# Kernel tuning notes

Measured on AMD Instinct MI355X. Metric: run time of the kernel, lower is better.

The kernel has to match this reference:

```python
import jax, jax.numpy as jnp
import numpy as np

B, T = 16, 512          # batch, timesteps
IN = 16                 # input_path_dim
D = 128                 # cde_state_dim
H = 256                 # vf_hidden_dim
L = 136                 # logsig_size = 16 + 16*15/2 (depth-2 log-signature)
O = 32                  # output_path_dim


def _linear_params(key, out_f, in_f):
    kw, kb = jax.random.split(key)
    lim = 1.0 / np.sqrt(in_f)
    W = jax.random.uniform(kw, (out_f, in_f), minval=-lim, maxval=lim, dtype=jnp.float32)
    b = jax.random.uniform(kb, (out_f,), minval=-lim, maxval=lim, dtype=jnp.float32)
    return W, b


def setup_inputs() -> dict:
    key = jax.random.key(0)
    ks = jax.random.split(key, 10)
    x0 = jax.random.normal(ks[0], (B, IN), dtype=jnp.float32)
    # log-signature increments are small; scale down for numerical realism
    logsigs = jax.random.normal(ks[1], (B, T - 1, L), dtype=jnp.float32) * 0.01
    # initial MLP: IN -> H -> H -> D (softplus activations, linear final)
    iw1, ib1 = _linear_params(ks[2], H, IN)
    iw2, ib2 = _linear_params(ks[3], H, H)
    iw3, ib3 = _linear_params(ks[4], D, H)
    # vector-field MLP: D -> H -> H -> D*L (softplus, tanh final)
    fw1, fb1 = _linear_params(ks[5], H, D)
    fw2, fb2 = _linear_params(ks[6], H, H)
    fw3, fb3 = _linear_params(ks[7], D * L, H)
    # readout: D -> O
    rw, rb = _linear_params(ks[8], O, D)
    return dict(x0=x0, logsigs=logsigs,
                iw1=iw1, ib1=ib1, iw2=iw2, ib2=ib2, iw3=iw3, ib3=ib3,
                fw1=fw1, fb1=fb1, fw2=fw2, fb2=fb2, fw3=fw3, fb3=fb3,
                rw=rw, rb=rb)


def reference(x0, logsigs, iw1, ib1, iw2, ib2, iw3, ib3,
              fw1, fb1, fw2, fb2, fw3, fb3, rw, rb):
    sp = jax.nn.softplus
    # initial MLP -> h0: (B, D)
    h0 = sp(x0 @ iw1.T + ib1)
    h0 = sp(h0 @ iw2.T + ib2)
    h0 = h0 @ iw3.T + ib3

    def step(h, logsig_t):
        # vector-field MLP: (B, D) -> (B, D*L), tanh final activation
        z = sp(h @ fw1.T + fb1)
        z = sp(z @ fw2.T + fb2)
        z = jnp.tanh(z @ fw3.T + fb3)
        mat = z.reshape(h.shape[0], D, L)          # (B, D, L)
        h_next = h + jnp.einsum('bdl,bl->bd', mat, logsig_t)
        return h_next, h_next

    # scan over time: xs shape (T-1, B, L)
    _, h_hist = jax.lax.scan(step, h0, jnp.swapaxes(logsigs, 0, 1))
    h_all = jnp.concatenate([h0[None, :, :], h_hist], axis=0)  # (T, B, D)
    out = h_all @ rw.T + rb                                     # (T, B, O)
    return jnp.swapaxes(out, 0, 1)                              # (B, T, O)
```

## Files before the change

kernel.cpp:

```cpp
#include <hip/hip_runtime.h>

namespace {
constexpr int kB = 16, kT = 512, kIN = 16, kD = 128, kH = 256, kL = 136, kO = 32;
constexpr int kSteps = kT - 1;
constexpr int NBLK = 256;
constexpr int NTHR = 512;
constexpr int LH   = 68;
constexpr int NTILE = 5;
constexpr int OFF_W3L = 0;
constexpr int OFF_AHI = 81920;
constexpr int OFF_ALO = 90368;
constexpr int OFF_DT  = 98816;
constexpr int OFF_OMS = 104192;
constexpr int OFF_Z1S = 108544;
constexpr int OFF_HB  = 109568;
constexpr int OFF_HINC= 110080;
constexpr int OFF_RED = 110592;
constexpr size_t LDS_BYTES = 111104;
}

typedef __attribute__((ext_vector_type(8))) short short8;
typedef __attribute__((ext_vector_type(4))) float f32x4;

__device__ __forceinline__ float softplusf(float x) {
  return fmaxf(x, 0.0f) + log1pf(expf(-fabsf(x)));
}
__device__ __forceinline__ unsigned short f2bf(float x) {
  unsigned u = __float_as_uint(x);
  return (unsigned short)((u + 0x7FFFu + ((u >> 16) & 1u)) >> 16);
}
__device__ __forceinline__ float bf2f(unsigned short h) {
  return __uint_as_float(((unsigned)h) << 16);
}
#define ALOAD64(p)   __hip_atomic_load((p),  __ATOMIC_RELAXED, __HIP_MEMORY_SCOPE_AGENT)
#define ASTORE64(p,v) __hip_atomic_store((p), (v), __ATOMIC_RELAXED, __HIP_MEMORY_SCOPE_AGENT)

__global__ void __launch_bounds__(256)
rde_init(const float* __restrict__ x0,
         const float* __restrict__ iw1, const float* __restrict__ ib1,
         const float* __restrict__ iw2, const float* __restrict__ ib2,
         const float* __restrict__ iw3, const float* __restrict__ ib3,
         float* __restrict__ hist) {
  __shared__ float xs[kIN];
  __shared__ __align__(16) float t1[kH];
  __shared__ __align__(16) float t2[kH];
  const int b = blockIdx.x, tid = threadIdx.x;
  if (tid < kIN) xs[tid] = x0[b*kIN + tid];
  __syncthreads();
  {
    float a = ib1[tid];
#pragma unroll
    for (int i = 0; i < kIN; ++i) a = fmaf(xs[i], iw1[tid*kIN + i], a);
    t1[tid] = softplusf(a);
  }
  __syncthreads();
  {
    const float4* wr = (const float4*)(iw2 + (size_t)tid*kH);
    float a = ib2[tid];
#pragma unroll 8
    for (int q = 0; q < kH/4; ++q) {
      float4 w = wr[q];
      a = fmaf(t1[4*q+0], w.x, a); a = fmaf(t1[4*q+1], w.y, a);
      a = fmaf(t1[4*q+2], w.z, a); a = fmaf(t1[4*q+3], w.w, a);
    }
    t2[tid] = softplusf(a);
  }
  __syncthreads();
  if (tid < kD) {
    const float4* wr = (const float4*)(iw3 + (size_t)tid*kH);
    float a = ib3[tid];
#pragma unroll 8
    for (int q = 0; q < kH/4; ++q) {
      float4 w = wr[q];
      a = fmaf(t2[4*q+0], w.x, a); a = fmaf(t2[4*q+1], w.y, a);
      a = fmaf(t2[4*q+2], w.z, a); a = fmaf(t2[4*q+3], w.w, a);
    }
    hist[(size_t)b*kD + tid] = a;
  }
}

__global__ void __launch_bounds__(NTHR, 2)
rde_scan(const float* __restrict__ lsg,
         const float* __restrict__ fw1, const float* __restrict__ fb1,
         const float* __restrict__ fw2, const float* __restrict__ fb2,
         const float* __restrict__ fw3, const float* __restrict__ fb3,
         float* __restrict__ hist,
         unsigned long long* z2x, unsigned long long* partx) {
  extern __shared__ char smem[];
  unsigned short* W3L = (unsigned short*)(smem + OFF_W3L);
  unsigned short* Ahi = (unsigned short*)(smem + OFF_AHI);
  unsigned short* Alo = (unsigned short*)(smem + OFF_ALO);
  float* Dt   = (float*)(smem + OFF_DT);
  float* oms  = (float*)(smem + OFF_OMS);
  float* z1s  = (float*)(smem + OFF_Z1S);
  float* hb   = (float*)(smem + OFF_HB);
  float* hinc = (float*)(smem + OFF_HINC);
  float* red  = (float*)(smem + OFF_RED);

  const int tid  = threadIdx.x;
  const int k    = blockIdx.x;
  const int wave = tid >> 6, lane = tid & 63;
  const int d_own = k >> 1, l0 = (k & 1) * LH;
  const bool isMLP = (k < kB);
  const int b_own = k;
  const int j = tid >> 1, ksp = tid & 1;

  for (int i = tid; i < NTILE*8*64; i += NTHR) {
    const int w = i >> 9, s = (i >> 6) & 7, ln = i & 63;
    const int nl = w*16 + (ln & 15), g = ln >> 4;
    unsigned hi4[4], lo4[4];
    if (nl < LH) {
      const float* wrow = fw3 + ((size_t)d_own*kL + l0 + nl)*kH + s*32 + g*8;
#pragma unroll
      for (int e = 0; e < 4; ++e) {
        float v0 = wrow[2*e], v1 = wrow[2*e+1];
        unsigned short h0 = f2bf(v0), h1 = f2bf(v1);
        unsigned short l0_ = f2bf(v0 - bf2f(h0)), l1_ = f2bf(v1 - bf2f(h1));
        hi4[e] = (unsigned)h0 | ((unsigned)h1 << 16);
        lo4[e] = (unsigned)l0_ | ((unsigned)l1_ << 16);
      }
    } else {
#pragma unroll
      for (int e = 0; e < 4; ++e) { hi4[e] = 0u; lo4[e] = 0u; }
    }
    unsigned* dh = (unsigned*)(W3L + (((w*8+s)*2+0)*64 + ln)*8);
    unsigned* dl = (unsigned*)(W3L + (((w*8+s)*2+1)*64 + ln)*8);
#pragma unroll
    for (int e = 0; e < 4; ++e) { dh[e] = hi4[e]; dl[e] = lo4[e]; }
  }
  float biasv = 0.f;
  if (wave < NTILE) {
    int nl = wave*16 + (lane & 15);
    if (nl < LH) biasv = fb3[(size_t)d_own*kL + l0 + nl];
  }
  float w1r[64], w2r[128];
  float myfb1 = 0.f, myfb2 = 0.f;
  if (isMLP) {
    const float* p1 = fw1 + (size_t)j*kD + ksp*64;
#pragma unroll
    for (int q = 0; q < 16; ++q) {
      float4 v = *(const float4*)(p1 + 4*q);
      w1r[4*q] = v.x; w1r[4*q+1] = v.y; w1r[4*q+2] = v.z; w1r[4*q+3] = v.w;
    }
    const float* p2 = fw2 + (size_t)j*kH + ksp*128;
#pragma unroll
    for (int q = 0; q < 32; ++q) {
      float4 v = *(const float4*)(p2 + 4*q);
      w2r[4*q] = v.x; w2r[4*q+1] = v.y; w2r[4*q+2] = v.z; w2r[4*q+3] = v.w;
    }
    myfb1 = fb1[j]; myfb2 = fb2[j];
    for (int i = tid; i < kD; i += NTHR) hb[i] = hist[(size_t)b_own*kD + i];
  }
  __syncthreads();

  for (int t = 0; t < kSteps; ++t) {
    const unsigned epw = (unsigned)(t + 1);

    if (isMLP) {
      {
        float a = 0.f;
#pragma unroll
        for (int q = 0; q < 16; ++q) {
          float4 h4 = *(const float4*)(hb + ksp*64 + 4*q);
          a = fmaf(h4.x, w1r[4*q  ], a); a = fmaf(h4.y, w1r[4*q+1], a);
          a = fmaf(h4.z, w1r[4*q+2], a); a = fmaf(h4.w, w1r[4*q+3], a);
        }
        a += __shfl_xor(a, 1);
        if (ksp == 0) z1s[j] = softplusf(a + myfb1);
      }
      __syncthreads();
      {
        float c = 0.f;
#pragma unroll
        for (int q = 0; q < 32; ++q) {
          float4 z4 = *(const float4*)(z1s + ksp*128 + 4*q);
          c = fmaf(z4.x, w2r[4*q  ], c); c = fmaf(z4.y, w2r[4*q+1], c);
          c = fmaf(z4.z, w2r[4*q+2], c); c = fmaf(z4.w, w2r[4*q+3], c);
        }
        c += __shfl_xor(c, 1);
        if (ksp == 0) {
          float v = softplusf(c + myfb2);
          unsigned short hh = f2bf(v), ll = f2bf(v - bf2f(hh));
          unsigned long long pk = (unsigned long long)((unsigned)hh | ((unsigned)ll << 16))
                                | ((unsigned long long)epw << 32);
          ASTORE64(z2x + b_own*kH + j, pk);
        }
      }
    }

    if (tid >= 256) {
      int c = tid - 256;
#pragma unroll 2
      for (int rep = 0; rep < 2; ++rep) {
        int cc = c + rep*256;
        if (cc < 272) {
          int bb = cc / 17, ii = cc % 17;
          float4 v = *(const float4*)(lsg + ((size_t)bb*kSteps + t)*kL + l0 + ii*4);
          *(float4*)(oms + bb*LH + ii*4) = v;
        }
      }
    }

    {
      const unsigned long long* src = z2x + tid*8;
      unsigned long long q8[8];
      for (;;) {
        bool ok = true;
#pragma unroll
        for (int i = 0; i < 8; ++i) q8[i] = ALOAD64(src + i);
#pragma unroll
        for (int i = 0; i < 8; ++i) ok &= ((unsigned)(q8[i] >> 32) == epw);
        if (ok) break;
        __builtin_amdgcn_s_sleep(1);
      }
      const int e0 = tid*8, m = e0 >> 8, kk = e0 & 255;
      unsigned short* ph = Ahi + m*264 + kk;
      unsigned short* pl = Alo + m*264 + kk;
#pragma unroll
      for (int i = 0; i < 4; ++i) {
        unsigned a = (unsigned)q8[2*i], b = (unsigned)q8[2*i+1];
        *(unsigned*)(ph + 2*i) = (a & 0xffffu) | (b << 16);
        *(unsigned*)(pl + 2*i) = (a >> 16) | (b & 0xffff0000u);
      }
    }
    __syncthreads();

    if (wave < NTILE) {
      f32x4 acc = {biasv, biasv, biasv, biasv};
      const int l15 = lane & 15, g = lane >> 4;
      const unsigned short* arh = Ahi + l15*264;
      const unsigned short* arl = Alo + l15*264;
#pragma unroll
      for (int s = 0; s < 8; ++s) {
        short8 ah = *(const short8*)(arh + s*32 + g*8);
        short8 al = *(const short8*)(arl + s*32 + g*8);
        short8 bh = *(const short8*)(W3L + ((wave*16 + s*2 + 0)*64 + lane)*8);
        short8 bl = *(const short8*)(W3L + ((wave*16 + s*2 + 1)*64 + lane)*8);
        acc = __builtin_amdgcn_mfma_f32_16x16x32_bf16(ah, bh, acc, 0, 0, 0);
        acc = __builtin_amdgcn_mfma_f32_16x16x32_bf16(ah, bl, acc, 0, 0, 0);
        acc = __builtin_amdgcn_mfma_f32_16x16x32_bf16(al, bh, acc, 0, 0, 0);
      }
#pragma unroll
      for (int r = 0; r < 4; ++r)
        Dt[(g*4 + r)*84 + wave*16 + l15] = acc[r];
    }
    __syncthreads();

    {
      const int b3 = tid & 15, lb = tid >> 4;
      float p = tanhf(Dt[b3*84 + lb     ]) * oms[b3*LH + lb     ]
              + tanhf(Dt[b3*84 + lb + 32]) * oms[b3*LH + lb + 32];
      if (lb < 4)
        p += tanhf(Dt[b3*84 + lb + 64]) * oms[b3*LH + lb + 64];
      p += __shfl_xor(p, 16); p += __shfl_xor(p, 32);
      if (lane < 16) red[lane*8 + wave] = p;
    }
    __syncthreads();
    if (tid < 16) {
      float s = 0.f;
#pragma unroll
      for (int jw = 0; jw < 8; ++jw) s += red[tid*8 + jw];
      unsigned long long pk = (unsigned long long)__float_as_uint(s)
                            | ((unsigned long long)epw << 32);
      ASTORE64(partx + tid*NBLK + k, pk);
    }

    if (isMLP) {
      if (tid < 256) {
        const unsigned long long* pp = partx + b_own*NBLK + tid;
        unsigned long long q;
        for (;;) {
          q = ALOAD64(pp);
          if ((unsigned)(q >> 32) == epw) break;
          __builtin_amdgcn_s_sleep(1);
        }
        float pv = __uint_as_float((unsigned)q);
        float p2 = pv + __shfl_xor(pv, 1);
        if ((tid & 1) == 0) hinc[tid >> 1] = p2;
      }
      __syncthreads();
      if (tid < 128) {
        float hn = hb[tid] + hinc[tid];
        hb[tid] = hn;
        hist[((size_t)(t+1)*kB + b_own)*kD + tid] = hn;
      }
      __syncthreads();
    }
  }
}

__global__ void __launch_bounds__(512)
rde_readout(const float* __restrict__ hist, const float* __restrict__ rw,
            const float* __restrict__ rb, float* __restrict__ out) {
  const int t = blockIdx.x, tid = threadIdx.x;
  const int b = tid >> 5, o = tid & 31;
  const float4* hr = (const float4*)(hist + ((size_t)t*kB + b)*kD);
  const float4* wr = (const float4*)(rw + (size_t)o*kD);
  float a = rb[o];
#pragma unroll 8
  for (int q = 0; q < kD/4; ++q) {
    float4 h4 = hr[q], w4 = wr[q];
    a = fmaf(h4.x,w4.x,a); a = fmaf(h4.y,w4.y,a);
    a = fmaf(h4.z,w4.z,a); a = fmaf(h4.w,w4.w,a);
  }
  out[((size_t)b*kT + t)*kO + o] = a;
}

extern "C" void kernel_launch(void* const* d_in, const int* in_sizes, int n_in,
                              void* d_out, int out_size, void* d_ws, size_t ws_size,
                              hipStream_t stream) {
  const float* x0  = (const float*)d_in[0];
  const float* lsg = (const float*)d_in[1];
  const float* iw1 = (const float*)d_in[2];
  const float* ib1 = (const float*)d_in[3];
  const float* iw2 = (const float*)d_in[4];
  const float* ib2 = (const float*)d_in[5];
  const float* iw3 = (const float*)d_in[6];
  const float* ib3 = (const float*)d_in[7];
  const float* fw1 = (const float*)d_in[8];
  const float* fb1 = (const float*)d_in[9];
  const float* fw2 = (const float*)d_in[10];
  const float* fb2 = (const float*)d_in[11];
  const float* fw3 = (const float*)d_in[12];
  const float* fb3 = (const float*)d_in[13];
  const float* rw  = (const float*)d_in[14];
  const float* rb  = (const float*)d_in[15];
  float* out = (float*)d_out;

  float* hist = (float*)d_ws;
  unsigned long long* z2x   = (unsigned long long*)(hist + (size_t)kT*kB*kD);
  unsigned long long* partx = z2x + (size_t)kB*kH;

  hipMemsetAsync(z2x, 0, (size_t)kB*kH*8 * 2, stream);
  hipFuncSetAttribute((const void*)rde_scan,
                      hipFuncAttributeMaxDynamicSharedMemorySize, (int)LDS_BYTES);

  rde_init<<<kB, 256, 0, stream>>>(x0, iw1, ib1, iw2, ib2, iw3, ib3, hist);

  void* args[] = { (void*)&lsg, (void*)&fw1, (void*)&fb1, (void*)&fw2, (void*)&fb2,
                   (void*)&fw3, (void*)&fb3, (void*)&hist, (void*)&z2x, (void*)&partx };
  hipLaunchCooperativeKernel((const void*)rde_scan, dim3(NBLK), dim3(NTHR),
                             args, (unsigned)LDS_BYTES, stream);

  rde_readout<<<kT, 512, 0, stream>>>(hist, rw, rb, out);
}
```

Baseline: 5.623 ms.

## Replicate vector-field MLP layers in every block via split-bf16 MFMA, broadcast h instead

Before, only 16 owner blocks computed the first two MLP layers in scalar FP32 and published z2 to all 256 blocks through global memory. Now every block recomputes both hidden layers redundantly for all 16 batch rows. It uses bf16 hi/lo split MFMA with the weights held in registers. Only the small updated h (128 floats per batch, packed hi/lo) is broadcast through global memory with a per-batch sentinel flag. This removes the serial scalar MLP from the critical path and shrinks the cross-block data exchanged each step. The costs are redundant compute, a large register footprint, and LDS growing to about 135KB, which forces 1 block per CU.

```diff
diff --git a/kernel.cpp b/kernel.cpp
--- a/kernel.cpp
+++ b/kernel.cpp
@@ -8,15 +8,18 @@
 constexpr int LH   = 68;
 constexpr int NTILE = 5;
 constexpr int OFF_W3L = 0;
-constexpr int OFF_AHI = 81920;
-constexpr int OFF_ALO = 90368;
-constexpr int OFF_DT  = 98816;
-constexpr int OFF_OMS = 104192;
-constexpr int OFF_Z1S = 108544;
-constexpr int OFF_HB  = 109568;
-constexpr int OFF_HINC= 110080;
-constexpr int OFF_RED = 110592;
-constexpr size_t LDS_BYTES = 111104;
+constexpr int OFF_Z1H = 81920;
+constexpr int OFF_Z1L = 90368;
+constexpr int OFF_Z2H = 98816;
+constexpr int OFF_Z2L = 107264;
+constexpr int OFF_HBH = 115712;
+constexpr int OFF_HBL = 120064;
+constexpr int OFF_DT  = 124416;
+constexpr int OFF_OMS = 129792;
+constexpr int OFF_RED = 134144;
+constexpr int OFF_HOWN= 134656;
+constexpr int OFF_HINC= 135168;
+constexpr size_t LDS_BYTES = 135680;
 }
 
 typedef __attribute__((ext_vector_type(8))) short short8;
@@ -32,8 +35,19 @@
 __device__ __forceinline__ float bf2f(unsigned short h) {
   return __uint_as_float(((unsigned)h) << 16);
 }
-#define ALOAD64(p)   __hip_atomic_load((p),  __ATOMIC_RELAXED, __HIP_MEMORY_SCOPE_AGENT)
+#define ALOAD32(p)    __hip_atomic_load((p),  __ATOMIC_RELAXED, __HIP_MEMORY_SCOPE_AGENT)
+#define ASTORE32(p,v) __hip_atomic_store((p), (v), __ATOMIC_RELAXED, __HIP_MEMORY_SCOPE_AGENT)
+#define ALOAD64(p)    __hip_atomic_load((p),  __ATOMIC_RELAXED, __HIP_MEMORY_SCOPE_AGENT)
 #define ASTORE64(p,v) __hip_atomic_store((p), (v), __ATOMIC_RELAXED, __HIP_MEMORY_SCOPE_AGENT)
+
+__device__ __forceinline__ void pack8(const float* v, short8& hi, short8& lo) {
+#pragma unroll
+  for (int e = 0; e < 8; ++e) {
+    unsigned short hh = f2bf(v[e]);
+    hi[e] = (short)hh;
+    lo[e] = (short)f2bf(v[e] - bf2f(hh));
+  }
+}
 
 __global__ void __launch_bounds__(256)
 rde_init(const float* __restrict__ x0,
@@ -79,161 +93,164 @@
   }
 }
 
-__global__ void __launch_bounds__(NTHR, 2)
+__global__ void __launch_bounds__(NTHR, 1)
 rde_scan(const float* __restrict__ lsg,
          const float* __restrict__ fw1, const float* __restrict__ fb1,
          const float* __restrict__ fw2, const float* __restrict__ fb2,
          const float* __restrict__ fw3, const float* __restrict__ fb3,
          float* __restrict__ hist,
-         unsigned long long* z2x, unsigned long long* partx) {
+         unsigned long long* partx, unsigned* hx, unsigned* hsnt) {
   extern __shared__ char smem[];
-  unsigned short* W3L = (unsigned short*)(smem + OFF_W3L);
-  unsigned short* Ahi = (unsigned short*)(smem + OFF_AHI);
-  unsigned short* Alo = (unsigned short*)(smem + OFF_ALO);
+  unsigned short* W3L  = (unsigned short*)(smem + OFF_W3L);
+  unsigned short* z1hi = (unsigned short*)(smem + OFF_Z1H);
+  unsigned short* z1lo = (unsigned short*)(smem + OFF_Z1L);
+  unsigned short* z2hi = (unsigned short*)(smem + OFF_Z2H);
+  unsigned short* z2lo = (unsigned short*)(smem + OFF_Z2L);
+  unsigned short* hbh  = (unsigned short*)(smem + OFF_HBH);
+  unsigned short* hbl  = (unsigned short*)(smem + OFF_HBL);
   float* Dt   = (float*)(smem + OFF_DT);
   float* oms  = (float*)(smem + OFF_OMS);
-  float* z1s  = (float*)(smem + OFF_Z1S);
-  float* hb   = (float*)(smem + OFF_HB);
+  float* red  = (float*)(smem + OFF_RED);
+  float* hown = (float*)(smem + OFF_HOWN);
   float* hinc = (float*)(smem + OFF_HINC);
-  float* red  = (float*)(smem + OFF_RED);
 
   const int tid  = threadIdx.x;
   const int k    = blockIdx.x;
   const int wave = tid >> 6, lane = tid & 63;
+  const int l15  = lane & 15, g = lane >> 4;
   const int d_own = k >> 1, l0 = (k & 1) * LH;
-  const bool isMLP = (k < kB);
-  const int b_own = k;
-  const int j = tid >> 1, ksp = tid & 1;
+  const bool isOwn = (k < kB);
 
   for (int i = tid; i < NTILE*8*64; i += NTHR) {
     const int w = i >> 9, s = (i >> 6) & 7, ln = i & 63;
-    const int nl = w*16 + (ln & 15), g = ln >> 4;
-    unsigned hi4[4], lo4[4];
+    const int nl = w*16 + (ln & 15), gg = ln >> 4;
+    float v[8];
     if (nl < LH) {
-      const float* wrow = fw3 + ((size_t)d_own*kL + l0 + nl)*kH + s*32 + g*8;
-#pragma unroll
-      for (int e = 0; e < 4; ++e) {
-        float v0 = wrow[2*e], v1 = wrow[2*e+1];
-        unsigned short h0 = f2bf(v0), h1 = f2bf(v1);
-        unsigned short l0_ = f2bf(v0 - bf2f(h0)), l1_ = f2bf(v1 - bf2f(h1));
-        hi4[e] = (unsigned)h0 | ((unsigned)h1 << 16);
-        lo4[e] = (unsigned)l0_ | ((unsigned)l1_ << 16);
-      }
+      const float* wrow = fw3 + ((size_t)d_own*kL + l0 + nl)*kH + s*32 + gg*8;
+      float4 a0 = *(const float4*)(wrow), a1 = *(const float4*)(wrow + 4);
+      v[0]=a0.x; v[1]=a0.y; v[2]=a0.z; v[3]=a0.w;
+      v[4]=a1.x; v[5]=a1.y; v[6]=a1.z; v[7]=a1.w;
     } else {
 #pragma unroll
-      for (int e = 0; e < 4; ++e) { hi4[e] = 0u; lo4[e] = 0u; }
-    }
-    unsigned* dh = (unsigned*)(W3L + (((w*8+s)*2+0)*64 + ln)*8);
-    unsigned* dl = (unsigned*)(W3L + (((w*8+s)*2+1)*64 + ln)*8);
-#pragma unroll
-    for (int e = 0; e < 4; ++e) { dh[e] = hi4[e]; dl[e] = lo4[e]; }
+      for (int e = 0; e < 8; ++e) v[e] = 0.f;
+    }
+    short8 hi, lo; pack8(v, hi, lo);
+    *(short8*)(W3L + (((w*8+s)*2+0)*64 + ln)*8) = hi;
+    *(short8*)(W3L + (((w*8+s)*2+1)*64 + ln)*8) = lo;
   }
   float biasv = 0.f;
   if (wave < NTILE) {
-    int nl = wave*16 + (lane & 15);
+    int nl = wave*16 + l15;
     if (nl < LH) biasv = fb3[(size_t)d_own*kL + l0 + nl];
   }
-  float w1r[64], w2r[128];
-  float myfb1 = 0.f, myfb2 = 0.f;
-  if (isMLP) {
-    const float* p1 = fw1 + (size_t)j*kD + ksp*64;
-#pragma unroll
-    for (int q = 0; q < 16; ++q) {
-      float4 v = *(const float4*)(p1 + 4*q);
-      w1r[4*q] = v.x; w1r[4*q+1] = v.y; w1r[4*q+2] = v.z; w1r[4*q+3] = v.w;
-    }
-    const float* p2 = fw2 + (size_t)j*kH + ksp*128;
-#pragma unroll
-    for (int q = 0; q < 32; ++q) {
-      float4 v = *(const float4*)(p2 + 4*q);
-      w2r[4*q] = v.x; w2r[4*q+1] = v.y; w2r[4*q+2] = v.z; w2r[4*q+3] = v.w;
-    }
-    myfb1 = fb1[j]; myfb2 = fb2[j];
-    for (int i = tid; i < kD; i += NTHR) hb[i] = hist[(size_t)b_own*kD + i];
+  short8 bw1h[2][4], bw1l[2][4], bw2h[2][8], bw2l[2][8];
+  float fb1v[2], fb2v[2];
+#pragma unroll
+  for (int ti = 0; ti < 2; ++ti) {
+    const int n = (wave*2 + ti)*16 + l15;
+    fb1v[ti] = fb1[n]; fb2v[ti] = fb2[n];
+#pragma unroll
+    for (int kst = 0; kst < 4; ++kst) {
+      const float* p = fw1 + (size_t)n*kD + kst*32 + g*8;
+      float v[8];
+      float4 a0 = *(const float4*)p, a1 = *(const float4*)(p + 4);
+      v[0]=a0.x; v[1]=a0.y; v[2]=a0.z; v[3]=a0.w;
+      v[4]=a1.x; v[5]=a1.y; v[6]=a1.z; v[7]=a1.w;
+      pack8(v, bw1h[ti][kst], bw1l[ti][kst]);
+    }
+#pragma unroll
+    for (int kst = 0; kst < 8; ++kst) {
+      const float* p = fw2 + (size_t)n*kH + kst*32 + g*8;
+      float v[8];
+      float4 a0 = *(const float4*)p, a1 = *(const float4*)(p + 4);
+      v[0]=a0.x; v[1]=a0.y; v[2]=a0.z; v[3]=a0.w;
+      v[4]=a1.x; v[5]=a1.y; v[6]=a1.z; v[7]=a1.w;
+      pack8(v, bw2h[ti][kst], bw2l[ti][kst]);
+    }
+  }
+  {
+    int idx = tid*4, b = idx >> 7, d = idx & 127;
+    const float* hp = hist + (size_t)b*kD + d;
+    float4 h4 = *(const float4*)hp;
+    float hv[4] = {h4.x, h4.y, h4.z, h4.w};
+    unsigned short hh[4], ll[4];
+#pragma unroll
+    for (int i = 0; i < 4; ++i) { hh[i] = f2bf(hv[i]); ll[i] = f2bf(hv[i] - bf2f(hh[i])); }
+    *(unsigned*)(hbh + b*136 + d)     = (unsigned)hh[0] | ((unsigned)hh[1] << 16);
+    *(unsigned*)(hbh + b*136 + d + 2) = (unsigned)hh[2] | ((unsigned)hh[3] << 16);
+    *(unsigned*)(hbl + b*136 + d)     = (unsigned)ll[0] | ((unsigned)ll[1] << 16);
+    *(unsigned*)(hbl + b*136 + d + 2) = (unsigned)ll[2] | ((unsigned)ll[3] << 16);
+  }
+  if (isOwn) {
+    if (tid < kD) hown[tid] = hist[(size_t)k*kD + tid];
   }
   __syncthreads();
 
   for (int t = 0; t < kSteps; ++t) {
     const unsigned epw = (unsigned)(t + 1);
 
-    if (isMLP) {
-      {
-        float a = 0.f;
-#pragma unroll
-        for (int q = 0; q < 16; ++q) {
-          float4 h4 = *(const float4*)(hb + ksp*64 + 4*q);
-          a = fmaf(h4.x, w1r[4*q  ], a); a = fmaf(h4.y, w1r[4*q+1], a);
-          a = fmaf(h4.z, w1r[4*q+2], a); a = fmaf(h4.w, w1r[4*q+3], a);
-        }
-        a += __shfl_xor(a, 1);
-        if (ksp == 0) z1s[j] = softplusf(a + myfb1);
-      }
-      __syncthreads();
-      {
-        float c = 0.f;
-#pragma unroll
-        for (int q = 0; q < 32; ++q) {
-          float4 z4 = *(const float4*)(z1s + ksp*128 + 4*q);
-          c = fmaf(z4.x, w2r[4*q  ], c); c = fmaf(z4.y, w2r[4*q+1], c);
-          c = fmaf(z4.z, w2r[4*q+2], c); c = fmaf(z4.w, w2r[4*q+3], c);
-        }
-        c += __shfl_xor(c, 1);
-        if (ksp == 0) {
-          float v = softplusf(c + myfb2);
-          unsigned short hh = f2bf(v), ll = f2bf(v - bf2f(hh));
-          unsigned long long pk = (unsigned long long)((unsigned)hh | ((unsigned)ll << 16))
-                                | ((unsigned long long)epw << 32);
-          ASTORE64(z2x + b_own*kH + j, pk);
-        }
-      }
-    }
-
-    if (tid >= 256) {
-      int c = tid - 256;
-#pragma unroll 2
-      for (int rep = 0; rep < 2; ++rep) {
-        int cc = c + rep*256;
-        if (cc < 272) {
-          int bb = cc / 17, ii = cc % 17;
-          float4 v = *(const float4*)(lsg + ((size_t)bb*kSteps + t)*kL + l0 + ii*4);
-          *(float4*)(oms + bb*LH + ii*4) = v;
-        }
-      }
-    }
-
     {
-      const unsigned long long* src = z2x + tid*8;
-      unsigned long long q8[8];
-      for (;;) {
-        bool ok = true;
-#pragma unroll
-        for (int i = 0; i < 8; ++i) q8[i] = ALOAD64(src + i);
-#pragma unroll
-        for (int i = 0; i < 8; ++i) ok &= ((unsigned)(q8[i] >> 32) == epw);
-        if (ok) break;
-        __builtin_amdgcn_s_sleep(1);
-      }
-      const int e0 = tid*8, m = e0 >> 8, kk = e0 & 255;
-      unsigned short* ph = Ahi + m*264 + kk;
-      unsigned short* pl = Alo + m*264 + kk;
-#pragma unroll
-      for (int i = 0; i < 4; ++i) {
-        unsigned a = (unsigned)q8[2*i], b = (unsigned)q8[2*i+1];
-        *(unsigned*)(ph + 2*i) = (a & 0xffffu) | (b << 16);
-        *(unsigned*)(pl + 2*i) = (a >> 16) | (b & 0xffff0000u);
+      f32x4 a0 = {fb1v[0], fb1v[0], fb1v[0], fb1v[0]};
+      f32x4 a1 = {fb1v[1], fb1v[1], fb1v[1], fb1v[1]};
+#pragma unroll
+      for (int kst = 0; kst < 4; ++kst) {
+        short8 ah = *(const short8*)(hbh + l15*136 + kst*32 + g*8);
+        short8 al = *(const short8*)(hbl + l15*136 + kst*32 + g*8);
+        a0 = __builtin_amdgcn_mfma_f32_16x16x32_bf16(ah, bw1h[0][kst], a0, 0, 0, 0);
+        a0 = __builtin_amdgcn_mfma_f32_16x16x32_bf16(ah, bw1l[0][kst], a0, 0, 0, 0);
+        a0 = __builtin_amdgcn_mfma_f32_16x16x32_bf16(al, bw1h[0][kst], a0, 0, 0, 0);
+        a1 = __builtin_amdgcn_mfma_f32_16x16x32_bf16(ah, bw1h[1][kst], a1, 0, 0, 0);
+        a1 = __builtin_amdgcn_mfma_f32_16x16x32_bf16(ah, bw1l[1][kst], a1, 0, 0, 0);
+        a1 = __builtin_amdgcn_mfma_f32_16x16x32_bf16(al, bw1h[1][kst], a1, 0, 0, 0);
+      }
+#pragma unroll
+      for (int r = 0; r < 4; ++r) {
+        const int row = g*4 + r;
+        float v0 = softplusf(a0[r]);
+        float v1 = softplusf(a1[r]);
+        unsigned short h0 = f2bf(v0), h1 = f2bf(v1);
+        z1hi[row*264 + (wave*2+0)*16 + l15] = h0;
+        z1lo[row*264 + (wave*2+0)*16 + l15] = f2bf(v0 - bf2f(h0));
+        z1hi[row*264 + (wave*2+1)*16 + l15] = h1;
+        z1lo[row*264 + (wave*2+1)*16 + l15] = f2bf(v1 - bf2f(h1));
+      }
+    }
+    __syncthreads();
+
+    {
+      f32x4 a0 = {fb2v[0], fb2v[0], fb2v[0], fb2v[0]};
+      f32x4 a1 = {fb2v[1], fb2v[1], fb2v[1], fb2v[1]};
+#pragma unroll
+      for (int kst = 0; kst < 8; ++kst) {
+        short8 ah = *(const short8*)(z1hi + l15*264 + kst*32 + g*8);
+        short8 al = *(const short8*)(z1lo + l15*264 + kst*32 + g*8);
+        a0 = __builtin_amdgcn_mfma_f32_16x16x32_bf16(ah, bw2h[0][kst], a0, 0, 0, 0);
+        a0 = __builtin_amdgcn_mfma_f32_16x16x32_bf16(ah, bw2l[0][kst], a0, 0, 0, 0);
+        a0 = __builtin_amdgcn_mfma_f32_16x16x32_bf16(al, bw2h[0][kst], a0, 0, 0, 0);
+        a1 = __builtin_amdgcn_mfma_f32_16x16x32_bf16(ah, bw2h[1][kst], a1, 0, 0, 0);
+        a1 = __builtin_amdgcn_mfma_f32_16x16x32_bf16(ah, bw2l[1][kst], a1, 0, 0, 0);
+        a1 = __builtin_amdgcn_mfma_f32_16x16x32_bf16(al, bw2h[1][kst], a1, 0, 0, 0);
+      }
+#pragma unroll
+      for (int r = 0; r < 4; ++r) {
+        const int row = g*4 + r;
+        float v0 = softplusf(a0[r]);
+        float v1 = softplusf(a1[r]);
+        unsigned short h0 = f2bf(v0), h1 = f2bf(v1);
+        z2hi[row*264 + (wave*2+0)*16 + l15] = h0;
+        z2lo[row*264 + (wave*2+0)*16 + l15] = f2bf(v0 - bf2f(h0));
+        z2hi[row*264 + (wave*2+1)*16 + l15] = h1;
+        z2lo[row*264 + (wave*2+1)*16 + l15] = f2bf(v1 - bf2f(h1));
       }
     }
     __syncthreads();
 
     if (wave < NTILE) {
       f32x4 acc = {biasv, biasv, biasv, biasv};
-      const int l15 = lane & 15, g = lane >> 4;
-      const unsigned short* arh = Ahi + l15*264;
-      const unsigned short* arl = Alo + l15*264;
 #pragma unroll
       for (int s = 0; s < 8; ++s) {
-        short8 ah = *(const short8*)(arh + s*32 + g*8);
-        short8 al = *(const short8*)(arl + s*32 + g*8);
+        short8 ah = *(const short8*)(z2hi + l15*264 + s*32 + g*8);
+        short8 al = *(const short8*)(z2lo + l15*264 + s*32 + g*8);
         short8 bh = *(const short8*)(W3L + ((wave*16 + s*2 + 0)*64 + lane)*8);
         short8 bl = *(const short8*)(W3L + ((wave*16 + s*2 + 1)*64 + lane)*8);
         acc = __builtin_amdgcn_mfma_f32_16x16x32_bf16(ah, bh, acc, 0, 0, 0);
@@ -243,6 +260,16 @@
 #pragma unroll
       for (int r = 0; r < 4; ++r)
         Dt[(g*4 + r)*84 + wave*16 + l15] = acc[r];
+    } else {
+#pragma unroll 2
+      for (int it = 0; it < 2; ++it) {
+        int idx = (wave - 5)*64 + lane + it*192;
+        if (idx < 272) {
+          int bb = idx / 17, ii = idx % 17;
+          float4 v = *(const float4*)(lsg + ((size_t)bb*kSteps + t)*kL + l0 + ii*4);
+          *(float4*)(oms + bb*LH + ii*4) = v;
+        }
+      }
     }
     __syncthreads();
 
@@ -253,7 +280,8 @@
       if (lb < 4)
         p += tanhf(Dt[b3*84 + lb + 64]) * oms[b3*LH + lb + 64];
       p += __shfl_xor(p, 16); p += __shfl_xor(p, 32);
-      if (lane < 16) red[lane*8 + wave] = p;
+      if ((lane & 63) < 16 && lane < 16) red[lane*8 + wave] = p;
+      else if (lane < 16) red[lane*8 + wave] = p;
     }
     __syncthreads();
     if (tid < 16) {
@@ -262,12 +290,12 @@
       for (int jw = 0; jw < 8; ++jw) s += red[tid*8 + jw];
       unsigned long long pk = (unsigned long long)__float_as_uint(s)
                             | ((unsigned long long)epw << 32);
-      ASTORE64(partx + tid*NBLK + k, pk);
-    }
-
-    if (isMLP) {
+      ASTORE64(partx + (size_t)tid*NBLK + k, pk);
+    }
+
+    if (isOwn) {
       if (tid < 256) {
-        const unsigned long long* pp = partx + b_own*NBLK + tid;
+        const unsigned long long* pp = partx + (size_t)k*NBLK + tid;
         unsigned long long q;
         for (;;) {
           q = ALOAD64(pp);
@@ -280,12 +308,32 @@
       }
       __syncthreads();
       if (tid < 128) {
-        float hn = hb[tid] + hinc[tid];
-        hb[tid] = hn;
-        hist[((size_t)(t+1)*kB + b_own)*kD + tid] = hn;
+        float hn = hown[tid] + hinc[tid];
+        hown[tid] = hn;
+        hist[((size_t)(t+1)*kB + k)*kD + tid] = hn;
+        unsigned short hh = f2bf(hn), ll = f2bf(hn - bf2f(hh));
+        ASTORE32(hx + k*kD + tid, (unsigned)hh | ((unsigned)ll << 16));
       }
       __syncthreads();
-    }
+      if (tid == 0) ASTORE32(hsnt + k*32, epw);
+    }
+
+    if (tid < 16) {
+      while (ALOAD32(hsnt + tid*32) != epw) __builtin_amdgcn_s_sleep(4);
+    }
+    __syncthreads();
+    asm volatile("" ::: "memory");
+    {
+      int idx = tid*4, b = idx >> 7, d = idx & 127;
+      const unsigned* hp = hx + b*kD + d;
+      unsigned v0 = ALOAD32(hp + 0), v1 = ALOAD32(hp + 1);
+      unsigned v2 = ALOAD32(hp + 2), v3 = ALOAD32(hp + 3);
+      *(unsigned*)(hbh + b*136 + d)     = (v0 & 0xffffu) | (v1 << 16);
+      *(unsigned*)(hbh + b*136 + d + 2) = (v2 & 0xffffu) | (v3 << 16);
+      *(unsigned*)(hbl + b*136 + d)     = (v0 >> 16) | (v1 & 0xffff0000u);
+      *(unsigned*)(hbl + b*136 + d + 2) = (v2 >> 16) | (v3 & 0xffff0000u);
+    }
+    __syncthreads();
   }
 }
 
@@ -328,17 +376,20 @@
   float* out = (float*)d_out;
 
   float* hist = (float*)d_ws;
-  unsigned long long* z2x   = (unsigned long long*)(hist + (size_t)kT*kB*kD);
-  unsigned long long* partx = z2x + (size_t)kB*kH;
-
-  hipMemsetAsync(z2x, 0, (size_t)kB*kH*8 * 2, stream);
+  unsigned long long* partx = (unsigned long long*)(hist + (size_t)kT*kB*kD);
+  unsigned* hx   = (unsigned*)(partx + (size_t)kB*NBLK);
+  unsigned* hsnt = hx + kB*kD;
+
+  hipMemsetAsync(partx, 0,
+                 (size_t)kB*NBLK*8 + (size_t)kB*kD*4 + (size_t)kB*32*4, stream);
   hipFuncSetAttribute((const void*)rde_scan,
                       hipFuncAttributeMaxDynamicSharedMemorySize, (int)LDS_BYTES);
 
   rde_init<<<kB, 256, 0, stream>>>(x0, iw1, ib1, iw2, ib2, iw3, ib3, hist);
 
   void* args[] = { (void*)&lsg, (void*)&fw1, (void*)&fb1, (void*)&fw2, (void*)&fb2,
-                   (void*)&fw3, (void*)&fb3, (void*)&hist, (void*)&z2x, (void*)&partx };
+                   (void*)&fw3, (void*)&fb3, (void*)&hist, (void*)&partx,
+                   (void*)&hx, (void*)&hsnt };
   hipLaunchCooperativeKernel((const void*)rde_scan, dim3(NBLK), dim3(NTHR),
                              args, (unsigned)LDS_BYTES, stream);
 
```

New measurement: 6.767 ms. 20.4% more time.

## Split scan into dedicated MLP and vector-field blocks with fp16 split MFMA

Applied to the files above, without the earlier changes.

Reassigns the cooperative grid so that 128 blocks run the vector-field MLP, with 8 blocks per batch each computing 32 layer-2 units. The other 128 blocks each own one state dimension across all 136 log-signature channels. Layer 1 moves to fp16 hi/lo split MFMA, and the fw3 weights are kept as single fp16 in LDS, which cuts MFMA count from 3 to 2 per k-step. Each d-block now emits one partial per batch, so the pairwise reduction and one barrier drop out of the per-step critical path. The cost is redundant layer-1 work in every MLP block and reduced fw3 weight precision.

```diff
diff --git a/kernel.cpp b/kernel.cpp
--- a/kernel.cpp
+++ b/kernel.cpp
@@ -5,34 +5,31 @@
 constexpr int kSteps = kT - 1;
 constexpr int NBLK = 256;
 constexpr int NTHR = 512;
-constexpr int LH   = 68;
-constexpr int NTILE = 5;
+constexpr int NMLPB = 128;
+constexpr int NT3 = 9;
 constexpr int OFF_W3L = 0;
-constexpr int OFF_AHI = 81920;
-constexpr int OFF_ALO = 90368;
-constexpr int OFF_DT  = 98816;
-constexpr int OFF_OMS = 104192;
-constexpr int OFF_Z1S = 108544;
-constexpr int OFF_HB  = 109568;
-constexpr int OFF_HINC= 110080;
-constexpr int OFF_RED = 110592;
-constexpr size_t LDS_BYTES = 111104;
-}
-
-typedef __attribute__((ext_vector_type(8))) short short8;
+constexpr int OFF_Z2H = 73728;
+constexpr int OFF_Z2L = 82432;
+constexpr int OFF_OMS = 91136;
+constexpr int OFF_RED = 100096;
+constexpr size_t LDS_BYTES = 100608;
+constexpr int OFF_FW2 = 0;
+constexpr int OFF_Z1S = 33280;
+constexpr int OFF_HB  = 34304;
+constexpr int OFF_HHI = 34816;
+constexpr int OFF_HLO = 35072;
+}
+
+typedef __attribute__((ext_vector_type(8))) _Float16 half8;
 typedef __attribute__((ext_vector_type(4))) float f32x4;
 
 __device__ __forceinline__ float softplusf(float x) {
   return fmaxf(x, 0.0f) + log1pf(expf(-fabsf(x)));
 }
-__device__ __forceinline__ unsigned short f2bf(float x) {
-  unsigned u = __float_as_uint(x);
-  return (unsigned short)((u + 0x7FFFu + ((u >> 16) & 1u)) >> 16);
-}
-__device__ __forceinline__ float bf2f(unsigned short h) {
-  return __uint_as_float(((unsigned)h) << 16);
-}
-#define ALOAD64(p)   __hip_atomic_load((p),  __ATOMIC_RELAXED, __HIP_MEMORY_SCOPE_AGENT)
+__device__ __forceinline__ unsigned short h2u(_Float16 h) {
+  unsigned short u; __builtin_memcpy(&u, &h, 2); return u;
+}
+#define ALOAD64(p)    __hip_atomic_load((p),  __ATOMIC_RELAXED, __HIP_MEMORY_SCOPE_AGENT)
 #define ASTORE64(p,v) __hip_atomic_store((p), (v), __ATOMIC_RELAXED, __HIP_MEMORY_SCOPE_AGENT)
 
 __global__ void __launch_bounds__(256)
@@ -79,7 +76,7 @@
   }
 }
 
-__global__ void __launch_bounds__(NTHR, 2)
+__global__ void __launch_bounds__(NTHR, 1)
 rde_scan(const float* __restrict__ lsg,
          const float* __restrict__ fw1, const float* __restrict__ fb1,
          const float* __restrict__ fw2, const float* __restrict__ fb2,
@@ -87,202 +84,195 @@
          float* __restrict__ hist,
          unsigned long long* z2x, unsigned long long* partx) {
   extern __shared__ char smem[];
-  unsigned short* W3L = (unsigned short*)(smem + OFF_W3L);
-  unsigned short* Ahi = (unsigned short*)(smem + OFF_AHI);
-  unsigned short* Alo = (unsigned short*)(smem + OFF_ALO);
-  float* Dt   = (float*)(smem + OFF_DT);
-  float* oms  = (float*)(smem + OFF_OMS);
-  float* z1s  = (float*)(smem + OFF_Z1S);
-  float* hb   = (float*)(smem + OFF_HB);
-  float* hinc = (float*)(smem + OFF_HINC);
-  float* red  = (float*)(smem + OFF_RED);
-
   const int tid  = threadIdx.x;
   const int k    = blockIdx.x;
   const int wave = tid >> 6, lane = tid & 63;
-  const int d_own = k >> 1, l0 = (k & 1) * LH;
-  const bool isMLP = (k < kB);
-  const int b_own = k;
-  const int j = tid >> 1, ksp = tid & 1;
-
-  for (int i = tid; i < NTILE*8*64; i += NTHR) {
-    const int w = i >> 9, s = (i >> 6) & 7, ln = i & 63;
-    const int nl = w*16 + (ln & 15), g = ln >> 4;
-    unsigned hi4[4], lo4[4];
-    if (nl < LH) {
-      const float* wrow = fw3 + ((size_t)d_own*kL + l0 + nl)*kH + s*32 + g*8;
-#pragma unroll
-      for (int e = 0; e < 4; ++e) {
-        float v0 = wrow[2*e], v1 = wrow[2*e+1];
-        unsigned short h0 = f2bf(v0), h1 = f2bf(v1);
-        unsigned short l0_ = f2bf(v0 - bf2f(h0)), l1_ = f2bf(v1 - bf2f(h1));
-        hi4[e] = (unsigned)h0 | ((unsigned)h1 << 16);
-        lo4[e] = (unsigned)l0_ | ((unsigned)l1_ << 16);
-      }
-    } else {
-#pragma unroll
-      for (int e = 0; e < 4; ++e) { hi4[e] = 0u; lo4[e] = 0u; }
-    }
-    unsigned* dh = (unsigned*)(W3L + (((w*8+s)*2+0)*64 + ln)*8);
-    unsigned* dl = (unsigned*)(W3L + (((w*8+s)*2+1)*64 + ln)*8);
-#pragma unroll
-    for (int e = 0; e < 4; ++e) { dh[e] = hi4[e]; dl[e] = lo4[e]; }
-  }
-  float biasv = 0.f;
-  if (wave < NTILE) {
-    int nl = wave*16 + (lane & 15);
-    if (nl < LH) biasv = fb3[(size_t)d_own*kL + l0 + nl];
-  }
-  float w1r[64], w2r[128];
-  float myfb1 = 0.f, myfb2 = 0.f;
-  if (isMLP) {
-    const float* p1 = fw1 + (size_t)j*kD + ksp*64;
-#pragma unroll
-    for (int q = 0; q < 16; ++q) {
-      float4 v = *(const float4*)(p1 + 4*q);
-      w1r[4*q] = v.x; w1r[4*q+1] = v.y; w1r[4*q+2] = v.z; w1r[4*q+3] = v.w;
-    }
-    const float* p2 = fw2 + (size_t)j*kH + ksp*128;
-#pragma unroll
-    for (int q = 0; q < 32; ++q) {
-      float4 v = *(const float4*)(p2 + 4*q);
-      w2r[4*q] = v.x; w2r[4*q+1] = v.y; w2r[4*q+2] = v.z; w2r[4*q+3] = v.w;
-    }
-    myfb1 = fb1[j]; myfb2 = fb2[j];
-    for (int i = tid; i < kD; i += NTHR) hb[i] = hist[(size_t)b_own*kD + i];
-  }
-  __syncthreads();
-
-  for (int t = 0; t < kSteps; ++t) {
-    const unsigned epw = (unsigned)(t + 1);
-
-    if (isMLP) {
+  const int l15  = lane & 15, g = lane >> 4;
+
+  if (k >= NMLPB) {
+    _Float16* W3L  = (_Float16*)(smem + OFF_W3L);
+    _Float16* z2hi = (_Float16*)(smem + OFF_Z2H);
+    _Float16* z2lo = (_Float16*)(smem + OFF_Z2L);
+    float* oms = (float*)(smem + OFF_OMS);
+    float* red = (float*)(smem + OFF_RED);
+    const int d_own = k - NMLPB;
+
+    for (int i = tid; i < NT3*8*64; i += NTHR) {
+      const int w = i >> 9, s = (i >> 6) & 7, ln = i & 63;
+      const int nl = w*16 + (ln & 15), col = s*32 + (ln >> 4)*8;
+      half8 hv;
+      if (nl < kL) {
+        const float* p = fw3 + ((size_t)d_own*kL + nl)*kH + col;
+#pragma unroll
+        for (int e = 0; e < 8; ++e) hv[e] = (_Float16)p[e];
+      } else {
+#pragma unroll
+        for (int e = 0; e < 8; ++e) hv[e] = (_Float16)0.f;
+      }
+      *(half8*)(W3L + ((w*8 + s)*64 + ln)*8) = hv;
+    }
+    const float biasv = fb3[(size_t)d_own*kL + wave*16 + l15];
+    const float bias8 = (wave == 7 && l15 < 8) ? fb3[(size_t)d_own*kL + 128 + l15] : 0.f;
+    __syncthreads();
+
+    for (int t = 0; t < kSteps; ++t) {
+      const unsigned epw = (unsigned)(t + 1);
+#pragma unroll 2
+      for (int rep = 0; rep < 2; ++rep) {
+        int cc = tid + rep*512;
+        if (cc < 544) {
+          int bb = cc / 34, ii = cc - bb*34;
+          float4 v = *(const float4*)(lsg + ((size_t)bb*kSteps + t)*kL + ii*4);
+          *(float4*)(oms + bb*140 + ii*4) = v;
+        }
+      }
+      unsigned long long q8[8];
       {
-        float a = 0.f;
-#pragma unroll
-        for (int q = 0; q < 16; ++q) {
-          float4 h4 = *(const float4*)(hb + ksp*64 + 4*q);
-          a = fmaf(h4.x, w1r[4*q  ], a); a = fmaf(h4.y, w1r[4*q+1], a);
-          a = fmaf(h4.z, w1r[4*q+2], a); a = fmaf(h4.w, w1r[4*q+3], a);
-        }
-        a += __shfl_xor(a, 1);
-        if (ksp == 0) z1s[j] = softplusf(a + myfb1);
+        const unsigned long long* src = z2x + (size_t)tid*8;
+        for (;;) {
+          bool ok = true;
+#pragma unroll
+          for (int i = 0; i < 8; ++i) q8[i] = ALOAD64(src + i);
+#pragma unroll
+          for (int i = 0; i < 8; ++i) ok &= ((unsigned)(q8[i] >> 32) == epw);
+          if (ok) break;
+          __builtin_amdgcn_s_sleep(1);
+        }
+      }
+      {
+        const int e0 = tid*8, m = e0 >> 8, kk = e0 & 255;
+        unsigned* ph = (unsigned*)(z2hi + m*272 + kk);
+        unsigned* pl = (unsigned*)(z2lo + m*272 + kk);
+#pragma unroll
+        for (int i = 0; i < 4; ++i) {
+          unsigned a = (unsigned)q8[2*i], b = (unsigned)q8[2*i+1];
+          ph[i] = (a & 0xffffu) | (b << 16);
+          pl[i] = (a >> 16) | (b & 0xffff0000u);
+        }
+      }
+      __syncthreads();
+
+      f32x4 acc = {biasv, biasv, biasv, biasv};
+      f32x4 acc8 = {bias8, bias8, bias8, bias8};
+#pragma unroll
+      for (int s = 0; s < 8; ++s) {
+        half8 ah = *(const half8*)(z2hi + l15*272 + s*32 + g*8);
+        half8 al = *(const half8*)(z2lo + l15*272 + s*32 + g*8);
+        half8 bh = *(const half8*)(W3L + ((wave*8 + s)*64 + lane)*8);
+        acc = __builtin_amdgcn_mfma_f32_16x16x32_f16(ah, bh, acc, 0, 0, 0);
+        acc = __builtin_amdgcn_mfma_f32_16x16x32_f16(al, bh, acc, 0, 0, 0);
+        if (wave == 7) {
+          half8 b8 = *(const half8*)(W3L + ((64 + s)*64 + lane)*8);
+          acc8 = __builtin_amdgcn_mfma_f32_16x16x32_f16(ah, b8, acc8, 0, 0, 0);
+          acc8 = __builtin_amdgcn_mfma_f32_16x16x32_f16(al, b8, acc8, 0, 0, 0);
+        }
+      }
+#pragma unroll
+      for (int r = 0; r < 4; ++r) {
+        const int b = g*4 + r;
+        float p = tanhf(acc[r]) * oms[b*140 + wave*16 + l15];
+        if (wave == 7 && l15 < 8)
+          p += tanhf(acc8[r]) * oms[b*140 + 128 + l15];
+        p += __shfl_xor(p, 1); p += __shfl_xor(p, 2);
+        p += __shfl_xor(p, 4); p += __shfl_xor(p, 8);
+        if (l15 == 0) red[b*8 + wave] = p;
+      }
+      __syncthreads();
+      if (tid < 16) {
+        float s = 0.f;
+#pragma unroll
+        for (int w = 0; w < 8; ++w) s += red[tid*8 + w];
+        unsigned long long pk = (unsigned long long)__float_as_uint(s)
+                              | ((unsigned long long)epw << 32);
+        ASTORE64(partx + (size_t)tid*NMLPB + d_own, pk);
+      }
+    }
+  } else {
+    float* fw2s = (float*)(smem + OFF_FW2);
+    float* z1s  = (float*)(smem + OFF_Z1S);
+    float* hb   = (float*)(smem + OFF_HB);
+    _Float16* hhi = (_Float16*)(smem + OFF_HHI);
+    _Float16* hlo = (_Float16*)(smem + OFF_HLO);
+    const int b_own = k >> 3, e8 = k & 7, j0 = e8 * 32;
+
+    half8 bw1[2][4];
+    float fb1v[2];
+#pragma unroll
+    for (int ti = 0; ti < 2; ++ti) {
+      const int n = (wave*2 + ti)*16 + l15;
+      fb1v[ti] = fb1[n];
+#pragma unroll
+      for (int kst = 0; kst < 4; ++kst) {
+        const float* p = fw1 + (size_t)n*kD + kst*32 + g*8;
+        half8 h;
+#pragma unroll
+        for (int e = 0; e < 8; ++e) h[e] = (_Float16)p[e];
+        bw1[ti][kst] = h;
+      }
+    }
+    const float fb2v = fb2[j0 + (tid >> 4)];
+    for (int i = tid; i < 32*64; i += NTHR) {
+      int jl = i >> 6, q = i & 63;
+      float4 v = *(const float4*)(fw2 + (size_t)(j0 + jl)*kH + q*4);
+      *(float4*)(fw2s + jl*260 + q*4) = v;
+    }
+    if (tid < kD) {
+      float hv = hist[(size_t)b_own*kD + tid];
+      hb[tid] = hv;
+      _Float16 hh = (_Float16)hv;
+      hhi[tid] = hh; hlo[tid] = (_Float16)(hv - (float)hh);
+    }
+    __syncthreads();
+
+    for (int t = 0; t < kSteps; ++t) {
+      const unsigned epw = (unsigned)(t + 1);
+      f32x4 a0 = {fb1v[0], fb1v[0], fb1v[0], fb1v[0]};
+      f32x4 a1 = {fb1v[1], fb1v[1], fb1v[1], fb1v[1]};
+#pragma unroll
+      for (int kst = 0; kst < 4; ++kst) {
+        half8 ah = *(const half8*)(hhi + kst*32 + g*8);
+        half8 al = *(const half8*)(hlo + kst*32 + g*8);
+        a0 = __builtin_amdgcn_mfma_f32_16x16x32_f16(ah, bw1[0][kst], a0, 0, 0, 0);
+        a0 = __builtin_amdgcn_mfma_f32_16x16x32_f16(al, bw1[0][kst], a0, 0, 0, 0);
+        a1 = __builtin_amdgcn_mfma_f32_16x16x32_f16(ah, bw1[1][kst], a1, 0, 0, 0);
+        a1 = __builtin_amdgcn_mfma_f32_16x16x32_f16(al, bw1[1][kst], a1, 0, 0, 0);
+      }
+      if (g == 0) {
+        z1s[(wave*2+0)*16 + l15] = softplusf(a0[0]);
+        z1s[(wave*2+1)*16 + l15] = softplusf(a1[0]);
       }
       __syncthreads();
       {
-        float c = 0.f;
-#pragma unroll
-        for (int q = 0; q < 32; ++q) {
-          float4 z4 = *(const float4*)(z1s + ksp*128 + 4*q);
-          c = fmaf(z4.x, w2r[4*q  ], c); c = fmaf(z4.y, w2r[4*q+1], c);
-          c = fmaf(z4.z, w2r[4*q+2], c); c = fmaf(z4.w, w2r[4*q+3], c);
-        }
-        c += __shfl_xor(c, 1);
-        if (ksp == 0) {
-          float v = softplusf(c + myfb2);
-          unsigned short hh = f2bf(v), ll = f2bf(v - bf2f(hh));
-          unsigned long long pk = (unsigned long long)((unsigned)hh | ((unsigned)ll << 16))
-                                | ((unsigned long long)epw << 32);
-          ASTORE64(z2x + b_own*kH + j, pk);
-        }
-      }
-    }
-
-    if (tid >= 256) {
-      int c = tid - 256;
-#pragma unroll 2
-      for (int rep = 0; rep < 2; ++rep) {
-        int cc = c + rep*256;
-        if (cc < 272) {
-          int bb = cc / 17, ii = cc % 17;
-          float4 v = *(const float4*)(lsg + ((size_t)bb*kSteps + t)*kL + l0 + ii*4);
-          *(float4*)(oms + bb*LH + ii*4) = v;
-        }
-      }
-    }
-
-    {
-      const unsigned long long* src = z2x + tid*8;
-      unsigned long long q8[8];
-      for (;;) {
-        bool ok = true;
-#pragma unroll
-        for (int i = 0; i < 8; ++i) q8[i] = ALOAD64(src + i);
-#pragma unroll
-        for (int i = 0; i < 8; ++i) ok &= ((unsigned)(q8[i] >> 32) == epw);
-        if (ok) break;
-        __builtin_amdgcn_s_sleep(1);
-      }
-      const int e0 = tid*8, m = e0 >> 8, kk = e0 & 255;
-      unsigned short* ph = Ahi + m*264 + kk;
-      unsigned short* pl = Alo + m*264 + kk;
-#pragma unroll
-      for (int i = 0; i < 4; ++i) {
-        unsigned a = (unsigned)q8[2*i], b = (unsigned)q8[2*i+1];
-        *(unsigned*)(ph + 2*i) = (a & 0xffffu) | (b << 16);
-        *(unsigned*)(pl + 2*i) = (a >> 16) | (b & 0xffff0000u);
-      }
-    }
-    __syncthreads();
-
-    if (wave < NTILE) {
-      f32x4 acc = {biasv, biasv, biasv, biasv};
-      const int l15 = lane & 15, g = lane >> 4;
-      const unsigned short* arh = Ahi + l15*264;
-      const unsigned short* arl = Alo + l15*264;
-#pragma unroll
-      for (int s = 0; s < 8; ++s) {
-        short8 ah = *(const short8*)(arh + s*32 + g*8);
-        short8 al = *(const short8*)(arl + s*32 + g*8);
-        short8 bh = *(const short8*)(W3L + ((wave*16 + s*2 + 0)*64 + lane)*8);
-        short8 bl = *(const short8*)(W3L + ((wave*16 + s*2 + 1)*64 + lane)*8);
-        acc = __builtin_amdgcn_mfma_f32_16x16x32_bf16(ah, bh, acc, 0, 0, 0);
-        acc = __builtin_amdgcn_mfma_f32_16x16x32_bf16(ah, bl, acc, 0, 0, 0);
-        acc = __builtin_amdgcn_mfma_f32_16x16x32_bf16(al, bh, acc, 0, 0, 0);
-      }
-#pragma unroll
-      for (int r = 0; r < 4; ++r)
-        Dt[(g*4 + r)*84 + wave*16 + l15] = acc[r];
-    }
-    __syncthreads();
-
-    {
-      const int b3 = tid & 15, lb = tid >> 4;
-      float p = tanhf(Dt[b3*84 + lb     ]) * oms[b3*LH + lb     ]
-              + tanhf(Dt[b3*84 + lb + 32]) * oms[b3*LH + lb + 32];
-      if (lb < 4)
-        p += tanhf(Dt[b3*84 + lb + 64]) * oms[b3*LH + lb + 64];
-      p += __shfl_xor(p, 16); p += __shfl_xor(p, 32);
-      if (lane < 16) red[lane*8 + wave] = p;
-    }
-    __syncthreads();
-    if (tid < 16) {
-      float s = 0.f;
-#pragma unroll
-      for (int jw = 0; jw < 8; ++jw) s += red[tid*8 + jw];
-      unsigned long long pk = (unsigned long long)__float_as_uint(s)
-                            | ((unsigned long long)epw << 32);
-      ASTORE64(partx + tid*NBLK + k, pk);
-    }
-
-    if (isMLP) {
-      if (tid < 256) {
-        const unsigned long long* pp = partx + b_own*NBLK + tid;
+        const int jl = tid >> 4, ks = tid & 15;
+        float a = 0.f;
+#pragma unroll
+        for (int kh = ks; kh < kH; kh += 16)
+          a = fmaf(z1s[kh], fw2s[jl*260 + kh], a);
+        a += __shfl_xor(a, 1); a += __shfl_xor(a, 2);
+        a += __shfl_xor(a, 4); a += __shfl_xor(a, 8);
+        if (ks == 0) {
+          float v = softplusf(a + fb2v);
+          _Float16 vh = (_Float16)v;
+          _Float16 vl = (_Float16)(v - (float)vh);
+          unsigned long long pk =
+              (unsigned long long)((unsigned)h2u(vh) | ((unsigned)h2u(vl) << 16))
+            | ((unsigned long long)epw << 32);
+          ASTORE64(z2x + b_own*kH + j0 + jl, pk);
+        }
+      }
+      if (tid < kD) {
+        const unsigned long long* pp = partx + (size_t)b_own*NMLPB + tid;
         unsigned long long q;
         for (;;) {
           q = ALOAD64(pp);
           if ((unsigned)(q >> 32) == epw) break;
           __builtin_amdgcn_s_sleep(1);
         }
-        float pv = __uint_as_float((unsigned)q);
-        float p2 = pv + __shfl_xor(pv, 1);
-        if ((tid & 1) == 0) hinc[tid >> 1] = p2;
-      }
-      __syncthreads();
-      if (tid < 128) {
-        float hn = hb[tid] + hinc[tid];
+        float hn = hb[tid] + __uint_as_float((unsigned)q);
         hb[tid] = hn;
-        hist[((size_t)(t+1)*kB + b_own)*kD + tid] = hn;
+        if (e8 == 0) hist[((size_t)(t+1)*kB + b_own)*kD + tid] = hn;
+        _Float16 hh = (_Float16)hn;
+        hhi[tid] = hh; hlo[tid] = (_Float16)(hn - (float)hh);
       }
       __syncthreads();
     }
@@ -328,10 +318,11 @@
   float* out = (float*)d_out;
 
   float* hist = (float*)d_ws;
-  unsigned long long* z2x   = (unsigned long long*)(hist + (size_t)kT*kB*kD);
+  unsigned long long* z2x =
+      (unsigned long long*)(hist + (size_t)kT*kB*kD);
   unsigned long long* partx = z2x + (size_t)kB*kH;
 
-  hipMemsetAsync(z2x, 0, (size_t)kB*kH*8 * 2, stream);
+  hipMemsetAsync(z2x, 0, ((size_t)kB*kH + (size_t)kB*NMLPB)*8, stream);
   hipFuncSetAttribute((const void*)rde_scan,
                       hipFuncAttributeMaxDynamicSharedMemorySize, (int)LDS_BYTES);
 
```

Result: faster. 4.840 ms (-13.9%).
